# Optimization experiments

Measured on AMD Instinct MI355X. Metric: run time of the kernel, lower is better.

Reference implementation:

```python
import jax, jax.numpy as jnp
import numpy as np

B, TC, TP = 2, 1024, 512
NVC, NVP = 8, 4
D, K, H, DFF, L, HOR, NQ = 128, 3, 8, 512, 2, 96, 3
DK = D // H
MASK_VAL = -1e4  # finite stand-in for -inf; entmax15 support never reaches entries this far below the row max


def entmax15(z):
    # Exact 1.5-entmax over the last axis (Peters & Martins sort-based algorithm).
    z = z / 2.0
    z = z - jnp.max(z, axis=-1, keepdims=True)
    zs = jnp.flip(jnp.sort(z, axis=-1), axis=-1)  # descending
    kk = jnp.arange(1, z.shape[-1] + 1, dtype=z.dtype)
    mean = jnp.cumsum(zs, axis=-1) / kk
    meansq = jnp.cumsum(zs * zs, axis=-1) / kk
    ss = kk * (meansq - mean * mean)
    delta = (1.0 - ss) / kk
    pos = delta > 0
    sqrt_d = jnp.where(pos, jnp.sqrt(jnp.where(pos, delta, 1.0)), 0.0)  # grad-safe sqrt
    tau = mean - sqrt_d
    support = jnp.sum((tau <= zs).astype(jnp.int32), axis=-1, keepdims=True)
    tau_star = jnp.take_along_axis(tau, support - 1, axis=-1)
    return jnp.square(jnp.clip(z - tau_star, 0.0, None))


def layer_norm(x, g, b, eps=1e-5):
    m = jnp.mean(x, axis=-1, keepdims=True)
    v = jnp.mean(jnp.square(x - m), axis=-1, keepdims=True)
    return (x - m) * jax.lax.rsqrt(v + eps) * g + b


def selector(x, conv_w, conv_b, sel_w, sel_b, key):
    # x: [B, T, nv]; causal depthwise-grouped conv -> per-var local states [B, T, nv, D]
    Bs, T, nv = x.shape
    xc = jnp.transpose(x, (0, 2, 1))  # [B, nv, T]
    out = jax.lax.conv_general_dilated(
        xc, conv_w, window_strides=(1,), padding=[(K - 1, 0)],
        dimension_numbers=('NCH', 'OIH', 'NCH'), feature_group_count=nv)
    ls = out.reshape(Bs, nv, D, T) + conv_b[None, :, :, None]
    ls = jnp.transpose(ls, (0, 3, 1, 2))  # [B, T, nv, D]
    scores = ls @ sel_w + sel_b  # [B, T, nv]
    scores = jnp.clip(scores, -10.0, 10.0)
    scores = scores + 1e-4 * jax.random.normal(key, scores.shape, scores.dtype)
    w = entmax15(scores)  # [B, T, nv]
    weighted = jnp.sum(ls * w[..., None], axis=2)  # [B, T, D]
    return weighted, w


def attn_block(x, Wq, bq, Wk, bk, Wv, bv, Wo, bo):
    Bs, T, _ = x.shape
    q = (x @ Wq + bq).reshape(Bs, T, H, DK)
    k = (x @ Wk + bk).reshape(Bs, T, H, DK)
    v = (x @ Wv + bv).reshape(Bs, T, H, DK)
    scores = jnp.einsum('bthd,bshd->bhts', q, k) / jnp.sqrt(jnp.float32(DK))
    mask = jnp.triu(jnp.ones((T, T), bool), 1)
    scores = jnp.where(mask[None, None], MASK_VAL, scores)
    w = entmax15(scores)            # [B, H, T, T]
    w_avg = jnp.mean(w, axis=1)     # [B, T, T]
    v_comb = jnp.mean(v, axis=2)    # [B, T, DK]
    out = jnp.einsum('bts,bsd->btd', w_avg, v_comb)
    return out @ Wo + bo, w_avg


def forward(x_cond, x_pred, cw_c, cb_c, sw_c, sb_c, cw_p, cb_p, sw_p, sb_p,
            Wq, bq, Wk, bk, Wv, bv, Wo, bo, ln1_g, ln1_b,
            fw1, fb1, fw2, fb2, ln2_g, ln2_b, proj_w, proj_b):
    nk = jax.random.key(42)
    xc, v_cond = selector(x_cond, cw_c, cb_c, sw_c, sb_c, jax.random.fold_in(nk, 0))
    xp, v_pred = selector(x_pred, cw_p, cb_p, sw_p, sb_p, jax.random.fold_in(nk, 1))
    x = jnp.concatenate([xc, xp], axis=1)  # [B, TC+TP, D]
    logs = []
    for l in range(L):
        a, w = attn_block(x, Wq[l], bq[l], Wk[l], bk[l], Wv[l], bv[l], Wo[l], bo[l])
        x = layer_norm(x + a, ln1_g[l], ln1_b[l])
        h = jax.nn.relu(x @ fw1[l] + fb1[l])
        x = layer_norm(h @ fw2[l] + fb2[l] + x, ln2_g[l], ln2_b[l])
        logs.append(w)
    seq_last = x[:, -1, :]
    out = jnp.einsum('bd,qdh->bqh', seq_last, proj_w) + proj_b  # [B, NQ, HOR]
    return out, v_cond, v_pred, jnp.stack(logs)


def setup_inputs():
    key = jax.random.key(0)
    ks = jax.random.split(key, 16)
    def w(i, shp):
        return (0.02 * jax.random.normal(ks[i], shp)).astype(jnp.float32)
    z = lambda shp: jnp.zeros(shp, jnp.float32)
    o = lambda shp: jnp.ones(shp, jnp.float32)
    return {
        'x_cond': jax.random.normal(ks[0], (B, TC, NVC), jnp.float32),
        'x_pred': jax.random.normal(ks[1], (B, TP, NVP), jnp.float32),
        'cw_c': w(2, (NVC * D, 1, K)), 'cb_c': z((NVC, D)),
        'sw_c': w(3, (D,)), 'sb_c': z((1,)),
        'cw_p': w(4, (NVP * D, 1, K)), 'cb_p': z((NVP, D)),
        'sw_p': w(5, (D,)), 'sb_p': z((1,)),
        'Wq': w(6, (L, D, D)), 'bq': z((L, D)),
        'Wk': w(7, (L, D, D)), 'bk': z((L, D)),
        'Wv': w(8, (L, D, D)), 'bv': z((L, D)),
        'Wo': w(9, (L, DK, D)), 'bo': z((L, D)),
        'ln1_g': o((L, D)), 'ln1_b': z((L, D)),
        'fw1': w(10, (L, D, DFF)), 'fb1': z((L, DFF)),
        'fw2': w(11, (L, DFF, D)), 'fb2': z((L, D)),
        'ln2_g': o((L, D)), 'ln2_b': z((L, D)),
        'proj_w': w(12, (NQ, D, HOR)), 'proj_b': z((NQ, HOR)),
    }


def reference(x_cond, x_pred, cw_c, cb_c, sw_c, sb_c, cw_p, cb_p, sw_p, sb_p,
              Wq, bq, Wk, bk, Wv, bv, Wo, bo, ln1_g, ln1_b,
              fw1, fb1, fw2, fb2, ln2_g, ln2_b, proj_w, proj_b):
    return forward(x_cond, x_pred, cw_c, cb_c, sw_c, sb_c, cw_p, cb_p, sw_p, sb_p,
                   Wq, bq, Wk, bk, Wv, bv, Wo, bo, ln1_g, ln1_b,
                   fw1, fb1, fw2, fb2, ln2_g, ln2_b, proj_w, proj_b)
```

## Files before the change

kernel.cpp:

```cpp
#include <hip/hip_runtime.h>

namespace {

constexpr int NB_  = 2;
constexpr int TC_  = 1024;
constexpr int TP_  = 512;
constexpr int TT_  = 1536;
constexpr int D_   = 128;
constexpr int H_   = 8;
constexpr int DK_  = 16;
constexpr int DFF_ = 512;
constexpr int L_   = 2;
constexpr int HOR_ = 96;
constexpr int NQ_  = 3;

constexpr int SCP_ = TT_ + 8;

typedef _Float16 h2 __attribute__((ext_vector_type(2)));

constexpr int OFF_OUT  = 0;
constexpr int OFF_VC   = NB_ * NQ_ * HOR_;
constexpr int OFF_VP   = OFF_VC + NB_ * TC_ * 8;
constexpr int OFF_LOGS = OFF_VP + NB_ * TP_ * 4;

constexpr int WS_XA  = 0;
constexpr int WS_XB  = WS_XA  + NB_ * TT_ * D_;
constexpr int WS_Q16 = WS_XB  + NB_ * TT_ * D_;
constexpr int WS_K16 = WS_Q16 + NB_ * TT_ * D_ / 2;
constexpr int WS_VC  = WS_K16 + NB_ * TT_ * D_ / 2;
constexpr int WS_WVC = WS_VC  + NB_ * TT_ * DK_;
constexpr int WS_BVC = WS_WVC + L_ * D_ * DK_;

__device__ inline unsigned short f2bf(float x) {
    unsigned u = __float_as_uint(x);
    u = (u + 0x7fffu + ((u >> 16) & 1u)) >> 16;
    return (unsigned short)u;
}
__device__ inline float bf2f_lo(unsigned dw) { return __uint_as_float(dw << 16); }
__device__ inline float bf2f_hi(unsigned dw) { return __uint_as_float(dw & 0xffff0000u); }

__device__ inline float dot2f(h2 a, h2 b, float c) {
#if __has_builtin(__builtin_amdgcn_fdot2)
    return __builtin_amdgcn_fdot2(a, b, c, false);
#else
    return c + (float)a[0] * (float)b[0] + (float)a[1] * (float)b[1];
#endif
}

template <int NV>
__device__ inline void selector_body(
    const float* __restrict__ x, const float* __restrict__ cw,
    const float* __restrict__ cb, const float* __restrict__ sw,
    const float* __restrict__ sb, float* __restrict__ vout,
    float* __restrict__ xout, int Tsel, int row_off, int blk)
{
    const int b = blk / Tsel;
    const int t = blk - b * Tsel;
    const int d = threadIdx.x;
    const int lane = d & 63, wave = d >> 6;

    __shared__ float wsum[2][NV];
    __shared__ float wls[NV];

    float xw[3 * NV];
    #pragma unroll
    for (int kk = 0; kk < 3; ++kk) {
        const int ts = t + kk - 2;
        #pragma unroll
        for (int v = 0; v < NV; ++v)
            xw[kk * NV + v] = (ts >= 0) ? x[((long)b * Tsel + ts) * NV + v] : 0.0f;
    }

    float ls[NV];
    #pragma unroll
    for (int v = 0; v < NV; ++v) {
        const float* cwp = cw + ((long)(v * D_ + d)) * 3;
        float a = cb[v * D_ + d];
        a = fmaf(xw[0 * NV + v], cwp[0], a);
        a = fmaf(xw[1 * NV + v], cwp[1], a);
        a = fmaf(xw[2 * NV + v], cwp[2], a);
        ls[v] = a;
    }

    {
        const float swd = sw[d];
        float p[NV];
        #pragma unroll
        for (int v = 0; v < NV; ++v) p[v] = ls[v] * swd;
        #pragma unroll
        for (int off = 32; off; off >>= 1) {
            #pragma unroll
            for (int v = 0; v < NV; ++v) p[v] += __shfl_xor(p[v], off);
        }
        if (lane == 0) {
            #pragma unroll
            for (int v = 0; v < NV; ++v) wsum[wave][v] = p[v];
        }
    }
    __syncthreads();

    if (d == 0) {
        float u[NV];
        float m = -1e30f;
        #pragma unroll
        for (int v = 0; v < NV; ++v) {
            float s = wsum[0][v] + wsum[1][v] + sb[0];
            s = fminf(fmaxf(s, -10.0f), 10.0f);
            u[v] = 0.5f * s;
            m = fmaxf(m, u[v]);
        }
        float tau = m - 1.0f;
        for (int it = 0; it < 12; ++it) {
            float S1 = 0.f, S2 = 0.f;
            #pragma unroll
            for (int v = 0; v < NV; ++v) {
                float dd = fmaxf(u[v] - tau, 0.f);
                S1 += dd; S2 = fmaf(dd, dd, S2);
            }
            tau += (S2 - 1.0f) / (2.0f * S1);
        }
        {
            float S1 = 0.f, S2 = 0.f, K = 0.f;
            #pragma unroll
            for (int v = 0; v < NV; ++v) {
                if (u[v] > tau) { S1 += u[v]; S2 = fmaf(u[v], u[v], S2); K += 1.f; }
            }
            const float mean = S1 / K;
            const float arg  = fmaxf(fmaf(mean, mean, -(S2 - 1.0f) / K), 0.f);
            tau = mean - sqrtf(arg);
        }
        #pragma unroll
        for (int v = 0; v < NV; ++v) {
            float dd = fmaxf(u[v] - tau, 0.f);
            wls[v] = dd * dd;
        }
    }
    __syncthreads();

    float acc = 0.f;
    #pragma unroll
    for (int v = 0; v < NV; ++v) acc = fmaf(ls[v], wls[v], acc);
    xout[((long)b * TT_ + row_off + t) * D_ + d] = acc;
    if (d < NV) vout[((long)b * Tsel + t) * NV + d] = wls[d];
}

__device__ inline void prep_body(
    const float* __restrict__ Wv, const float* __restrict__ bv,
    float* __restrict__ wvc, float* __restrict__ bvc, int l)
{
    const float* W  = Wv + (long)l * D_ * D_;
    const float* bb = bv + l * D_;
    float* wv = wvc + l * D_ * DK_;
    float* bo = bvc + l * DK_;
    const int tid = threadIdx.x;
    for (int idx = tid; idx < D_ * DK_; idx += 128) {
        const int i = idx >> 4, dk = idx & 15;
        float s = 0.f;
        #pragma unroll
        for (int hh = 0; hh < H_; ++hh) s += W[i * D_ + hh * DK_ + dk];
        wv[idx] = s * 0.125f;
    }
    if (tid < DK_) {
        float s = 0.f;
        #pragma unroll
        for (int hh = 0; hh < H_; ++hh) s += bb[hh * DK_ + tid];
        bo[tid] = s * 0.125f;
    }
}

__global__ __launch_bounds__(128) void pre_kernel(
    const float* __restrict__ x_cond, const float* __restrict__ cw_c,
    const float* __restrict__ cb_c, const float* __restrict__ sw_c,
    const float* __restrict__ sb_c,
    const float* __restrict__ x_pred, const float* __restrict__ cw_p,
    const float* __restrict__ cb_p, const float* __restrict__ sw_p,
    const float* __restrict__ sb_p,
    const float* __restrict__ Wv, const float* __restrict__ bv,
    float* __restrict__ vc_out, float* __restrict__ vp_out,
    float* __restrict__ xout, float* __restrict__ wvc,
    float* __restrict__ bvc)
{
    const int blk = blockIdx.x;
    if (blk < NB_ * TC_) {
        selector_body<8>(x_cond, cw_c, cb_c, sw_c, sb_c, vc_out, xout,
                         TC_, 0, blk);
    } else if (blk < NB_ * TC_ + NB_ * TP_) {
        selector_body<4>(x_pred, cw_p, cb_p, sw_p, sb_p, vp_out, xout,
                         TP_, TC_, blk - NB_ * TC_);
    } else {
        prep_body(Wv, bv, wvc, bvc, blk - (NB_ * TC_ + NB_ * TP_));
    }
}

__global__ __launch_bounds__(256) void qkv_kernel(
    const float* __restrict__ x,
    const float* __restrict__ Wq, const float* __restrict__ bq,
    const float* __restrict__ Wk, const float* __restrict__ bk,
    const float* __restrict__ wvc, const float* __restrict__ bvc,
    _Float16* __restrict__ q16, _Float16* __restrict__ k16,
    float* __restrict__ vc)
{
    __shared__ float xrT[D_][4];
    const long row0 = (long)blockIdx.x * 4;
    const int tid = threadIdx.x;

    for (int idx = tid; idx < 4 * D_; idx += 256) {
        const int r = idx >> 7, i = idx & 127;
        xrT[i][r] = x[row0 * D_ + idx];
    }
    __syncthreads();

    const int c = tid & 127;
    const int which = tid >> 7;
    const float* __restrict__ W = which ? Wk : Wq;
    const float bb = which ? bk[c] : bq[c];
    float a0 = bb, a1 = bb, a2 = bb, a3 = bb;
    for (int i = 0; i < D_; ++i) {
        const float wv = W[i * D_ + c];
        const float4 xv = *(const float4*)&xrT[i][0];
        a0 = fmaf(xv.x, wv, a0);
        a1 = fmaf(xv.y, wv, a1);
        a2 = fmaf(xv.z, wv, a2);
        a3 = fmaf(xv.w, wv, a3);
    }
    _Float16* __restrict__ dst = which ? k16 : q16;
    dst[(row0 + 0) * D_ + c] = (_Float16)a0;
    dst[(row0 + 1) * D_ + c] = (_Float16)a1;
    dst[(row0 + 2) * D_ + c] = (_Float16)a2;
    dst[(row0 + 3) * D_ + c] = (_Float16)a3;

    if (tid < 64) {
        const int r = tid >> 4, c16 = tid & 15;
        float av = bvc[c16];
        for (int i = 0; i < D_; ++i)
            av = fmaf(xrT[i][r], wvc[i * DK_ + c16], av);
        vc[(row0 + r) * DK_ + c16] = av;
    }
}

template <int NJ>
__device__ inline void entmax_head(unsigned short* __restrict__ srow,
                                   int lane, int t)
{
    const unsigned* __restrict__ rp = (const unsigned*)srow;
    unsigned dw[NJ];
    #pragma unroll
    for (int j = 0; j < NJ; ++j) dw[j] = rp[64 * j + lane];
    float v[2 * NJ];
    #pragma unroll
    for (int j = 0; j < NJ; ++j) {
        const int s0 = 128 * j + 2 * lane;
        v[2*j]   = (s0     <= t) ? bf2f_lo(dw[j]) : -1e30f;
        v[2*j+1] = (s0 + 1 <= t) ? bf2f_hi(dw[j]) : -1e30f;
    }

    float m = -1e30f;
    #pragma unroll
    for (int j = 0; j < 2 * NJ; ++j) m = fmaxf(m, v[j]);
    #pragma unroll
    for (int off = 32; off; off >>= 1) m = fmaxf(m, __shfl_xor(m, off));

    float tau = m - 1.0f;
    #pragma unroll
    for (int it = 0; it < 7; ++it) {
        float S1 = 0.f, S2 = 0.f;
        #pragma unroll
        for (int j = 0; j < 2 * NJ; ++j) {
            const float d0 = fmaxf(v[j] - tau, 0.f);
            S1 += d0; S2 = fmaf(d0, d0, S2);
        }
        #pragma unroll
        for (int off = 32; off; off >>= 1) {
            S1 += __shfl_xor(S1, off);
            S2 += __shfl_xor(S2, off);
        }
        tau += (S2 - 1.0f) / (2.0f * S1);
    }
    {
        float S1 = 0.f, S2 = 0.f, K = 0.f;
        #pragma unroll
        for (int j = 0; j < 2 * NJ; ++j) {
            if (v[j] > tau) { S1 += v[j]; S2 = fmaf(v[j], v[j], S2); K += 1.f; }
        }
        #pragma unroll
        for (int off = 32; off; off >>= 1) {
            S1 += __shfl_xor(S1, off);
            S2 += __shfl_xor(S2, off);
            K  += __shfl_xor(K,  off);
        }
        const float mean = S1 / K;
        const float arg  = fmaxf(fmaf(mean, mean, -(S2 - 1.0f) / K), 0.f);
        tau = mean - sqrtf(arg);
    }
    unsigned* __restrict__ wp = (unsigned*)srow;
    #pragma unroll
    for (int j = 0; j < NJ; ++j) {
        const float d0 = fmaxf(v[2*j]   - tau, 0.f);
        const float d1 = fmaxf(v[2*j+1] - tau, 0.f);
        const unsigned lo = f2bf(d0 * d0);
        const unsigned hi = f2bf(d1 * d1);
        wp[64 * j + lane] = lo | (hi << 16);
    }
    #pragma unroll
    for (int j = NJ; j < 12; ++j) wp[64 * j + lane] = 0;
}

template <int NJ>
__device__ inline void entmax_pair(unsigned short* __restrict__ scb,
                                   int wave, int lane, int t)
{
    entmax_head<NJ>(scb + (wave * 2 + 0) * SCP_, lane, t);
    entmax_head<NJ>(scb + (wave * 2 + 1) * SCP_, lane, t);
}

__global__ __launch_bounds__(256) void attn_kernel(
    const _Float16* __restrict__ q16, const _Float16* __restrict__ k16,
    const float* __restrict__ vcomb, const float* __restrict__ xin,
    float* __restrict__ xout,
    const float* __restrict__ Wo, const float* __restrict__ bo,
    const float* __restrict__ lng, const float* __restrict__ lnb,
    float* __restrict__ logs)
{
    __shared__ unsigned short scb[H_ * SCP_];
    __shared__ _Float16 qrow16[D_];
    __shared__ float red[64];
    __shared__ float o16[DK_];
    __shared__ float yrow[D_];
    __shared__ float stat[2];

    const int blk = blockIdx.x;
    const int t = TT_ - 1 - (blk >> 1);
    const int b = blk & 1;
    const int tid = threadIdx.x;
    const int lane = tid & 63, wave = tid >> 6;
    const long rowq  = (long)b * TT_ + t;
    const long bbase = (long)b * TT_;

    if (tid < 64)
        ((unsigned*)qrow16)[tid] = ((const unsigned*)(q16 + rowq * D_))[tid];
    __syncthreads();

    {
        const int h  = tid & 7;
        const int sl = tid >> 3;
        unsigned short* __restrict__ srow = scb + h * SCP_;
        h2 qv[8];
        __builtin_memcpy(qv, (const _Float16*)qrow16 + h * DK_, 32);
        for (int s = sl; s <= t; s += 32) {
            float4 kk0, kk1;
            {
                const float4* kp4 = (const float4*)(k16 + (bbase + s) * D_ + h * DK_);
                kk0 = kp4[0]; kk1 = kp4[1];
            }
            h2 kh[8];
            __builtin_memcpy(kh,     &kk0, 16);
            __builtin_memcpy(kh + 4, &kk1, 16);
            float dot = 0.f;
            #pragma unroll
            for (int i2 = 0; i2 < 8; ++i2) dot = dot2f(qv[i2], kh[i2], dot);
            srow[s] = f2bf(dot * 0.125f);
        }
    }
    __syncthreads();

    {
        const int njn = (t >> 7) + 1;
        switch ((njn + 1) & ~1) {
        case 2:  entmax_pair<2 >(scb, wave, lane, t); break;
        case 4:  entmax_pair<4 >(scb, wave, lane, t); break;
        case 6:  entmax_pair<6 >(scb, wave, lane, t); break;
        case 8:  entmax_pair<8 >(scb, wave, lane, t); break;
        case 10: entmax_pair<10>(scb, wave, lane, t); break;
        default: entmax_pair<12>(scb, wave, lane, t); break;
        }
    }
    __syncthreads();

    float4 A0 = make_float4(0,0,0,0), A1 = A0, A2 = A0, A3 = A0;
    float* lrow = logs + rowq * TT_;
    const unsigned* __restrict__ rp0 = (const unsigned*)scb;
    #pragma unroll
    for (int it = 0; it < 3; ++it) {
        const int dwi = tid + 256 * it;
        const int s0 = 2 * dwi;
        if (s0 <= t) {
            float wa0 = 0.f, wa1 = 0.f;
            #pragma unroll
            for (int h = 0; h < H_; ++h) {
                const unsigned d = rp0[h * (SCP_ / 2) + dwi];
                wa0 += bf2f_lo(d);
                wa1 += bf2f_hi(d);
            }
            wa0 *= 0.125f; wa1 *= 0.125f;
            {
                const float4* vp = (const float4*)(vcomb + (bbase + s0) * DK_);
                const float4 v0 = vp[0], v1 = vp[1], v2 = vp[2], v3 = vp[3];
                A0.x = fmaf(wa0, v0.x, A0.x); A0.y = fmaf(wa0, v0.y, A0.y);
                A0.z = fmaf(wa0, v0.z, A0.z); A0.w = fmaf(wa0, v0.w, A0.w);
                A1.x = fmaf(wa0, v1.x, A1.x); A1.y = fmaf(wa0, v1.y, A1.y);
                A1.z = fmaf(wa0, v1.z, A1.z); A1.w = fmaf(wa0, v1.w, A1.w);
                A2.x = fmaf(wa0, v2.x, A2.x); A2.y = fmaf(wa0, v2.y, A2.y);
                A2.z = fmaf(wa0, v2.z, A2.z); A2.w = fmaf(wa0, v2.w, A2.w);
                A3.x = fmaf(wa0, v3.x, A3.x); A3.y = fmaf(wa0, v3.y, A3.y);
                A3.z = fmaf(wa0, v3.z, A3.z); A3.w = fmaf(wa0, v3.w, A3.w);
            }
            if (s0 + 1 <= t) {
                const float4* vp = (const float4*)(vcomb + (bbase + s0 + 1) * DK_);
                const float4 v0 = vp[0], v1 = vp[1], v2 = vp[2], v3 = vp[3];
                A0.x = fmaf(wa1, v0.x, A0.x); A0.y = fmaf(wa1, v0.y, A0.y);
                A0.z = fmaf(wa1, v0.z, A0.z); A0.w = fmaf(wa1, v0.w, A0.w);
                A1.x = fmaf(wa1, v1.x, A1.x); A1.y = fmaf(wa1, v1.y, A1.y);
                A1.z = fmaf(wa1, v1.z, A1.z); A1.w = fmaf(wa1, v1.w, A1.w);
                A2.x = fmaf(wa1, v2.x, A2.x); A2.y = fmaf(wa1, v2.y, A2.y);
                A2.z = fmaf(wa1, v2.z, A2.z); A2.w = fmaf(wa1, v2.w, A2.w);
                A3.x = fmaf(wa1, v3.x, A3.x); A3.y = fmaf(wa1, v3.y, A3.y);
                A3.z = fmaf(wa1, v3.z, A3.z); A3.w = fmaf(wa1, v3.w, A3.w);
            }
            *(float2*)(lrow + s0) = make_float2(wa0, wa1);
        } else {
            *(float2*)(lrow + s0) = make_float2(0.f, 0.f);
        }
    }
    #pragma unroll
    for (int off = 32; off; off >>= 1) {
        A0.x += __shfl_xor(A0.x, off); A0.y += __shfl_xor(A0.y, off);
        A0.z += __shfl_xor(A0.z, off); A0.w += __shfl_xor(A0.w, off);
        A1.x += __shfl_xor(A1.x, off); A1.y += __shfl_xor(A1.y, off);
        A1.z += __shfl_xor(A1.z, off); A1.w += __shfl_xor(A1.w, off);
        A2.x += __shfl_xor(A2.x, off); A2.y += __shfl_xor(A2.y, off);
        A2.z += __shfl_xor(A2.z, off); A2.w += __shfl_xor(A2.w, off);
        A3.x += __shfl_xor(A3.x, off); A3.y += __shfl_xor(A3.y, off);
        A3.z += __shfl_xor(A3.z, off); A3.w += __shfl_xor(A3.w, off);
    }
    if (lane == 0) {
        float* r = red + wave * 16;
        r[0]=A0.x; r[1]=A0.y; r[2]=A0.z; r[3]=A0.w;
        r[4]=A1.x; r[5]=A1.y; r[6]=A1.z; r[7]=A1.w;
        r[8]=A2.x; r[9]=A2.y; r[10]=A2.z; r[11]=A2.w;
        r[12]=A3.x; r[13]=A3.y; r[14]=A3.z; r[15]=A3.w;
    }
    __syncthreads();
    if (tid < DK_) o16[tid] = red[tid] + red[16 + tid] + red[32 + tid] + red[48 + tid];
    __syncthreads();

    float y = 0.f;
    if (tid < D_) {
        float a = bo[tid];
        #pragma unroll
        for (int j = 0; j < DK_; ++j) a = fmaf(o16[j], Wo[j * D_ + tid], a);
        y = xin[rowq * D_ + tid] + a;
        yrow[tid] = y;
    }
    __syncthreads();
    if (tid < 64) {
        float sm = yrow[tid] + yrow[tid + 64];
        #pragma unroll
        for (int off = 32; off; off >>= 1) sm += __shfl_xor(sm, off);
        if (tid == 0) stat[0] = sm * (1.0f / D_);
    }
    __syncthreads();
    if (tid < 64) {
        const float mean = stat[0];
        const float d0 = yrow[tid] - mean, d1 = yrow[tid + 64] - mean;
        float sv = fmaf(d0, d0, d1 * d1);
        #pragma unroll
        for (int off = 32; off; off >>= 1) sv += __shfl_xor(sv, off);
        if (tid == 0) stat[1] = sv * (1.0f / D_);
    }
    __syncthreads();
    if (tid < D_) {
        const float r = rsqrtf(stat[1] + 1e-5f);
        xout[rowq * D_ + tid] = (y - stat[0]) * r * lng[tid] + lnb[tid];
    }
}

__global__ __launch_bounds__(256) void ffn_kernel(
    const float* __restrict__ xin, float* __restrict__ xout,
    const float* __restrict__ fw1, const float* __restrict__ fb1,
    const float* __restrict__ fw2, const float* __restrict__ fb2,
    const float* __restrict__ g, const float* __restrict__ bta,
    int do_proj, const float* __restrict__ pw,
    const float* __restrict__ pb, float* __restrict__ outp)
{
    __shared__ float xrT[D_][4];
    __shared__ float hbT[DFF_][4];
    __shared__ float yb[4][D_];
    __shared__ float xn[D_];

    const long row0 = (long)blockIdx.x * 4;
    const int tid = threadIdx.x;

    for (int idx = tid; idx < 4 * D_; idx += 256) {
        const int r = idx >> 7, i = idx & 127;
        xrT[i][r] = xin[row0 * D_ + idx];
    }
    __syncthreads();

    {
        const int c = tid;
        float4 a0 = make_float4(0,0,0,0), a1 = a0;
        for (int i = 0; i < D_; ++i) {
            const float w0 = fw1[i * DFF_ + c];
            const float w1 = fw1[i * DFF_ + c + 256];
            const float4 xv = *(const float4*)&xrT[i][0];
            a0.x = fmaf(xv.x, w0, a0.x); a0.y = fmaf(xv.y, w0, a0.y);
            a0.z = fmaf(xv.z, w0, a0.z); a0.w = fmaf(xv.w, w0, a0.w);
            a1.x = fmaf(xv.x, w1, a1.x); a1.y = fmaf(xv.y, w1, a1.y);
            a1.z = fmaf(xv.z, w1, a1.z); a1.w = fmaf(xv.w, w1, a1.w);
        }
        const float b0 = fb1[c], b1 = fb1[c + 256];
        float4 h0, h1;
        h0.x = fmaxf(a0.x + b0, 0.f); h0.y = fmaxf(a0.y + b0, 0.f);
        h0.z = fmaxf(a0.z + b0, 0.f); h0.w = fmaxf(a0.w + b0, 0.f);
        h1.x = fmaxf(a1.x + b1, 0.f); h1.y = fmaxf(a1.y + b1, 0.f);
        h1.z = fmaxf(a1.z + b1, 0.f); h1.w = fmaxf(a1.w + b1, 0.f);
        *(float4*)&hbT[c][0]       = h0;
        *(float4*)&hbT[c + 256][0] = h1;
    }
    __syncthreads();

    {
        const int d = tid & 127;
        const int r0 = (tid >> 7) * 2;
        float a0 = 0.f, a1 = 0.f;
        for (int j = 0; j < DFF_; ++j) {
            const float wv = fw2[j * D_ + d];
            const float2 hv = *(const float2*)&hbT[j][r0];
            a0 = fmaf(hv.x, wv, a0);
            a1 = fmaf(hv.y, wv, a1);
        }
        const float bb = fb2[d];
        yb[r0 + 0][d] = a0 + bb + xrT[d][r0 + 0];
        yb[r0 + 1][d] = a1 + bb + xrT[d][r0 + 1];
    }
    __syncthreads();

    const int w = tid >> 6, lane = tid & 63;
    const bool pblk = do_proj && (((row0 + 4) % TT_) == 0);
    {
        const float y0 = yb[w][lane], y1 = yb[w][lane + 64];
        float sm = y0 + y1;
        #pragma unroll
        for (int off = 32; off; off >>= 1) sm += __shfl_xor(sm, off);
        const float mean = sm * (1.0f / D_);
        const float d0 = y0 - mean, d1 = y1 - mean;
        float sv = fmaf(d0, d0, d1 * d1);
        #pragma unroll
        for (int off = 32; off; off >>= 1) sv += __shfl_xor(sv, off);
        const float rcp = rsqrtf(sv * (1.0f / D_) + 1e-5f);
        const float o0 = d0 * rcp * g[lane]      + bta[lane];
        const float o1 = d1 * rcp * g[lane + 64] + bta[lane + 64];
        xout[(row0 + w) * D_ + lane]      = o0;
        xout[(row0 + w) * D_ + lane + 64] = o1;
        if (pblk && w == 3) { xn[lane] = o0; xn[lane + 64] = o1; }
    }
    if (pblk) {
        __syncthreads();
        const int b = (int)((row0 + 3) / TT_);
        for (int idx = tid; idx < NQ_ * HOR_; idx += 256) {
            const int qq = idx / HOR_, hh = idx - qq * HOR_;
            float s = pb[idx];
            for (int d = 0; d < D_; ++d)
                s = fmaf(xn[d], pw[((long)qq * D_ + d) * HOR_ + hh], s);
            outp[b * NQ_ * HOR_ + idx] = s;
        }
    }
}

}

extern "C" void kernel_launch(void* const* d_in, const int* in_sizes, int n_in,
                              void* d_out, int out_size, void* d_ws, size_t ws_size,
                              hipStream_t stream) {
    (void)in_sizes; (void)n_in; (void)out_size; (void)ws_size;

    const float* x_cond = (const float*)d_in[0];
    const float* x_pred = (const float*)d_in[1];
    const float* cw_c   = (const float*)d_in[2];
    const float* cb_c   = (const float*)d_in[3];
    const float* sw_c   = (const float*)d_in[4];
    const float* sb_c   = (const float*)d_in[5];
    const float* cw_p   = (const float*)d_in[6];
    const float* cb_p   = (const float*)d_in[7];
    const float* sw_p   = (const float*)d_in[8];
    const float* sb_p   = (const float*)d_in[9];
    const float* Wq     = (const float*)d_in[10];
    const float* bq     = (const float*)d_in[11];
    const float* Wk     = (const float*)d_in[12];
    const float* bk     = (const float*)d_in[13];
    const float* Wv     = (const float*)d_in[14];
    const float* bv     = (const float*)d_in[15];
    const float* Wo     = (const float*)d_in[16];
    const float* bo     = (const float*)d_in[17];
    const float* ln1g   = (const float*)d_in[18];
    const float* ln1b   = (const float*)d_in[19];
    const float* fw1    = (const float*)d_in[20];
    const float* fb1    = (const float*)d_in[21];
    const float* fw2    = (const float*)d_in[22];
    const float* fb2    = (const float*)d_in[23];
    const float* ln2g   = (const float*)d_in[24];
    const float* ln2b   = (const float*)d_in[25];
    const float* pw     = (const float*)d_in[26];
    const float* pb     = (const float*)d_in[27];

    float* outp = (float*)d_out;
    float* ws   = (float*)d_ws;
    float*     xA   = ws + WS_XA;
    float*     xB   = ws + WS_XB;
    _Float16*  q16  = (_Float16*)(ws + WS_Q16);
    _Float16*  k16  = (_Float16*)(ws + WS_K16);
    float*     vcb  = ws + WS_VC;
    float*     wvc  = ws + WS_WVC;
    float*     bvc  = ws + WS_BVC;

    pre_kernel<<<NB_ * TC_ + NB_ * TP_ + L_, 128, 0, stream>>>(
        x_cond, cw_c, cb_c, sw_c, sb_c,
        x_pred, cw_p, cb_p, sw_p, sb_p,
        Wv, bv, outp + OFF_VC, outp + OFF_VP, xA, wvc, bvc);

    for (int l = 0; l < L_; ++l) {
        qkv_kernel<<<NB_ * TT_ / 4, 256, 0, stream>>>(
            xA, Wq + (long)l * D_ * D_, bq + l * D_,
            Wk + (long)l * D_ * D_, bk + l * D_,
            wvc + l * D_ * DK_, bvc + l * DK_, q16, k16, vcb);
        attn_kernel<<<NB_ * TT_, 256, 0, stream>>>(
            q16, k16, vcb, xA, xB,
            Wo + (long)l * DK_ * D_, bo + l * D_,
            ln1g + l * D_, ln1b + l * D_,
            outp + OFF_LOGS + (long)l * NB_ * TT_ * TT_);
        ffn_kernel<<<NB_ * TT_ / 4, 256, 0, stream>>>(
            xB, xA, fw1 + (long)l * D_ * DFF_, fb1 + l * DFF_,
            fw2 + (long)l * DFF_ * D_, fb2 + l * D_,
            ln2g + l * D_, ln2b + l * D_,
            (l == L_ - 1) ? 1 : 0, pw, pb, outp);
    }
}
```

Measured before the change: 342.1 us.

## Fuse QKV projection into selector and FFN kernels, dropping qkv_kernel launches

Removes the standalone qkv_kernel. The layer-0 Q/K/V projection now runs at the tail of the selector kernel, one row per block. The next layer's projection now runs at the tail of the FFN kernel, reusing the LayerNorm output already staged in shared memory. The Wv head-averaging prep moves into its own tiny kernel so the selector can depend on it. This saves launches and a re-read of the activations, but the selector path now reads the full Wq/Wk once per row instead of once per four rows, which lowers weight reuse.

```diff
diff --git a/kernel.cpp b/kernel.cpp
--- a/kernel.cpp
+++ b/kernel.cpp
@@ -47,12 +47,42 @@
 #endif
 }
 
+__global__ __launch_bounds__(128) void prep_wvc_kernel(
+    const float* __restrict__ Wv, const float* __restrict__ bv,
+    float* __restrict__ wvc, float* __restrict__ bvc)
+{
+    const int l = blockIdx.x;
+    const float* W  = Wv + (long)l * D_ * D_;
+    const float* bb = bv + l * D_;
+    float* wv = wvc + l * D_ * DK_;
+    float* bo = bvc + l * DK_;
+    const int tid = threadIdx.x;
+    for (int idx = tid; idx < D_ * DK_; idx += 128) {
+        const int i = idx >> 4, dk = idx & 15;
+        float s = 0.f;
+        #pragma unroll
+        for (int hh = 0; hh < H_; ++hh) s += W[i * D_ + hh * DK_ + dk];
+        wv[idx] = s * 0.125f;
+    }
+    if (tid < DK_) {
+        float s = 0.f;
+        #pragma unroll
+        for (int hh = 0; hh < H_; ++hh) s += bb[hh * DK_ + tid];
+        bo[tid] = s * 0.125f;
+    }
+}
+
 template <int NV>
 __device__ inline void selector_body(
     const float* __restrict__ x, const float* __restrict__ cw,
     const float* __restrict__ cb, const float* __restrict__ sw,
     const float* __restrict__ sb, float* __restrict__ vout,
-    float* __restrict__ xout, int Tsel, int row_off, int blk)
+    float* __restrict__ xout, int Tsel, int row_off, int blk,
+    const float* __restrict__ Wq, const float* __restrict__ bq,
+    const float* __restrict__ Wk, const float* __restrict__ bk,
+    const float* __restrict__ wvc, const float* __restrict__ bvc,
+    _Float16* __restrict__ q16, _Float16* __restrict__ k16,
+    float* __restrict__ vc)
 {
     const int b = blk / Tsel;
     const int t = blk - b * Tsel;
@@ -61,6 +91,8 @@
 
     __shared__ float wsum[2][NV];
     __shared__ float wls[NV];
+    __shared__ float xr[D_];
+    __shared__ float vred[DK_][8];
 
     float xw[3 * NV];
     #pragma unroll
@@ -140,31 +172,36 @@
     float acc = 0.f;
     #pragma unroll
     for (int v = 0; v < NV; ++v) acc = fmaf(ls[v], wls[v], acc);
-    xout[((long)b * TT_ + row_off + t) * D_ + d] = acc;
+    const long row = (long)b * TT_ + row_off + t;
+    xout[row * D_ + d] = acc;
     if (d < NV) vout[((long)b * Tsel + t) * NV + d] = wls[d];
-}
-
-__device__ inline void prep_body(
-    const float* __restrict__ Wv, const float* __restrict__ bv,
-    float* __restrict__ wvc, float* __restrict__ bvc, int l)
-{
-    const float* W  = Wv + (long)l * D_ * D_;
-    const float* bb = bv + l * D_;
-    float* wv = wvc + l * D_ * DK_;
-    float* bo = bvc + l * DK_;
-    const int tid = threadIdx.x;
-    for (int idx = tid; idx < D_ * DK_; idx += 128) {
-        const int i = idx >> 4, dk = idx & 15;
-        float s = 0.f;
-        #pragma unroll
-        for (int hh = 0; hh < H_; ++hh) s += W[i * D_ + hh * DK_ + dk];
-        wv[idx] = s * 0.125f;
-    }
-    if (tid < DK_) {
-        float s = 0.f;
-        #pragma unroll
-        for (int hh = 0; hh < H_; ++hh) s += bb[hh * DK_ + tid];
-        bo[tid] = s * 0.125f;
+
+    xr[d] = acc;
+    __syncthreads();
+
+    float aq = bq[d], ak = bk[d];
+    for (int i = 0; i < D_; ++i) {
+        const float xv = xr[i];
+        aq = fmaf(xv, Wq[i * D_ + d], aq);
+        ak = fmaf(xv, Wk[i * D_ + d], ak);
+    }
+    q16[row * D_ + d] = (_Float16)aq;
+    k16[row * D_ + d] = (_Float16)ak;
+
+    {
+        const int dk = d & 15, ch = d >> 4;
+        float p = 0.f;
+        #pragma unroll
+        for (int i = 0; i < 16; ++i)
+            p = fmaf(xr[ch * 16 + i], wvc[(ch * 16 + i) * DK_ + dk], p);
+        vred[dk][ch] = p;
+    }
+    __syncthreads();
+    if (d < DK_) {
+        float s = bvc[d];
+        #pragma unroll
+        for (int ch = 0; ch < 8; ++ch) s += vred[d][ch];
+        vc[row * DK_ + d] = s;
     }
 }
 
@@ -175,66 +212,22 @@
     const float* __restrict__ x_pred, const float* __restrict__ cw_p,
     const float* __restrict__ cb_p, const float* __restrict__ sw_p,
     const float* __restrict__ sb_p,
-    const float* __restrict__ Wv, const float* __restrict__ bv,
     float* __restrict__ vc_out, float* __restrict__ vp_out,
-    float* __restrict__ xout, float* __restrict__ wvc,
-    float* __restrict__ bvc)
-{
-    const int blk = blockIdx.x;
-    if (blk < NB_ * TC_) {
-        selector_body<8>(x_cond, cw_c, cb_c, sw_c, sb_c, vc_out, xout,
-                         TC_, 0, blk);
-    } else if (blk < NB_ * TC_ + NB_ * TP_) {
-        selector_body<4>(x_pred, cw_p, cb_p, sw_p, sb_p, vp_out, xout,
-                         TP_, TC_, blk - NB_ * TC_);
-    } else {
-        prep_body(Wv, bv, wvc, bvc, blk - (NB_ * TC_ + NB_ * TP_));
-    }
-}
-
-__global__ __launch_bounds__(256) void qkv_kernel(
-    const float* __restrict__ x,
+    float* __restrict__ xout,
     const float* __restrict__ Wq, const float* __restrict__ bq,
     const float* __restrict__ Wk, const float* __restrict__ bk,
     const float* __restrict__ wvc, const float* __restrict__ bvc,
     _Float16* __restrict__ q16, _Float16* __restrict__ k16,
     float* __restrict__ vc)
 {
-    __shared__ float xrT[D_][4];
-    const long row0 = (long)blockIdx.x * 4;
-    const int tid = threadIdx.x;
-
-    for (int idx = tid; idx < 4 * D_; idx += 256) {
-        const int r = idx >> 7, i = idx & 127;
-        xrT[i][r] = x[row0 * D_ + idx];
-    }
-    __syncthreads();
-
-    const int c = tid & 127;
-    const int which = tid >> 7;
-    const float* __restrict__ W = which ? Wk : Wq;
-    const float bb = which ? bk[c] : bq[c];
-    float a0 = bb, a1 = bb, a2 = bb, a3 = bb;
-    for (int i = 0; i < D_; ++i) {
-        const float wv = W[i * D_ + c];
-        const float4 xv = *(const float4*)&xrT[i][0];
-        a0 = fmaf(xv.x, wv, a0);
-        a1 = fmaf(xv.y, wv, a1);
-        a2 = fmaf(xv.z, wv, a2);
-        a3 = fmaf(xv.w, wv, a3);
-    }
-    _Float16* __restrict__ dst = which ? k16 : q16;
-    dst[(row0 + 0) * D_ + c] = (_Float16)a0;
-    dst[(row0 + 1) * D_ + c] = (_Float16)a1;
-    dst[(row0 + 2) * D_ + c] = (_Float16)a2;
-    dst[(row0 + 3) * D_ + c] = (_Float16)a3;
-
-    if (tid < 64) {
-        const int r = tid >> 4, c16 = tid & 15;
-        float av = bvc[c16];
-        for (int i = 0; i < D_; ++i)
-            av = fmaf(xrT[i][r], wvc[i * DK_ + c16], av);
-        vc[(row0 + r) * DK_ + c16] = av;
+    const int blk = blockIdx.x;
+    if (blk < NB_ * TC_) {
+        selector_body<8>(x_cond, cw_c, cb_c, sw_c, sb_c, vc_out, xout,
+                         TC_, 0, blk, Wq, bq, Wk, bk, wvc, bvc, q16, k16, vc);
+    } else {
+        selector_body<4>(x_pred, cw_p, cb_p, sw_p, sb_p, vp_out, xout,
+                         TP_, TC_, blk - NB_ * TC_,
+                         Wq, bq, Wk, bk, wvc, bvc, q16, k16, vc);
     }
 }
 
@@ -479,6 +472,12 @@
     const float* __restrict__ fw1, const float* __restrict__ fb1,
     const float* __restrict__ fw2, const float* __restrict__ fb2,
     const float* __restrict__ g, const float* __restrict__ bta,
+    int do_qkv,
+    const float* __restrict__ Wq, const float* __restrict__ bq,
+    const float* __restrict__ Wk, const float* __restrict__ bk,
+    const float* __restrict__ wvc, const float* __restrict__ bvc,
+    _Float16* __restrict__ q16, _Float16* __restrict__ k16,
+    float* __restrict__ vc,
     int do_proj, const float* __restrict__ pw,
     const float* __restrict__ pb, float* __restrict__ outp)
 {
@@ -552,8 +551,41 @@
         const float o1 = d1 * rcp * g[lane + 64] + bta[lane + 64];
         xout[(row0 + w) * D_ + lane]      = o0;
         xout[(row0 + w) * D_ + lane + 64] = o1;
+        xrT[lane][w]      = o0;
+        xrT[lane + 64][w] = o1;
         if (pblk && w == 3) { xn[lane] = o0; xn[lane + 64] = o1; }
     }
+
+    if (do_qkv) {
+        __syncthreads();
+        const int c = tid & 127;
+        const int which = tid >> 7;
+        const float* __restrict__ W = which ? Wk : Wq;
+        const float bb = which ? bk[c] : bq[c];
+        float a0 = bb, a1 = bb, a2 = bb, a3 = bb;
+        for (int i = 0; i < D_; ++i) {
+            const float wv = W[i * D_ + c];
+            const float4 xv = *(const float4*)&xrT[i][0];
+            a0 = fmaf(xv.x, wv, a0);
+            a1 = fmaf(xv.y, wv, a1);
+            a2 = fmaf(xv.z, wv, a2);
+            a3 = fmaf(xv.w, wv, a3);
+        }
+        _Float16* __restrict__ dst = which ? k16 : q16;
+        dst[(row0 + 0) * D_ + c] = (_Float16)a0;
+        dst[(row0 + 1) * D_ + c] = (_Float16)a1;
+        dst[(row0 + 2) * D_ + c] = (_Float16)a2;
+        dst[(row0 + 3) * D_ + c] = (_Float16)a3;
+
+        if (tid < 64) {
+            const int r = tid >> 4, c16 = tid & 15;
+            float av = bvc[c16];
+            for (int i = 0; i < D_; ++i)
+                av = fmaf(xrT[i][r], wvc[i * DK_ + c16], av);
+            vc[(row0 + r) * DK_ + c16] = av;
+        }
+    }
+
     if (pblk) {
         __syncthreads();
         const int b = (int)((row0 + 3) / TT_);
@@ -613,25 +645,33 @@
     float*     wvc  = ws + WS_WVC;
     float*     bvc  = ws + WS_BVC;
 
-    pre_kernel<<<NB_ * TC_ + NB_ * TP_ + L_, 128, 0, stream>>>(
+    prep_wvc_kernel<<<L_, 128, 0, stream>>>(Wv, bv, wvc, bvc);
+
+    pre_kernel<<<NB_ * TC_ + NB_ * TP_, 128, 0, stream>>>(
         x_cond, cw_c, cb_c, sw_c, sb_c,
         x_pred, cw_p, cb_p, sw_p, sb_p,
-        Wv, bv, outp + OFF_VC, outp + OFF_VP, xA, wvc, bvc);
+        outp + OFF_VC, outp + OFF_VP, xA,
+        Wq, bq, Wk, bk, wvc, bvc, q16, k16, vcb);
 
     for (int l = 0; l < L_; ++l) {
-        qkv_kernel<<<NB_ * TT_ / 4, 256, 0, stream>>>(
-            xA, Wq + (long)l * D_ * D_, bq + l * D_,
-            Wk + (long)l * D_ * D_, bk + l * D_,
-            wvc + l * D_ * DK_, bvc + l * DK_, q16, k16, vcb);
         attn_kernel<<<NB_ * TT_, 256, 0, stream>>>(
             q16, k16, vcb, xA, xB,
             Wo + (long)l * DK_ * D_, bo + l * D_,
             ln1g + l * D_, ln1b + l * D_,
             outp + OFF_LOGS + (long)l * NB_ * TT_ * TT_);
+        const int nl = l + 1;
         ffn_kernel<<<NB_ * TT_ / 4, 256, 0, stream>>>(
             xB, xA, fw1 + (long)l * D_ * DFF_, fb1 + l * DFF_,
             fw2 + (long)l * DFF_ * D_, fb2 + l * D_,
             ln2g + l * D_, ln2b + l * D_,
+            (l < L_ - 1) ? 1 : 0,
+            Wq + (long)nl * D_ * D_ * (l < L_ - 1),
+            bq + nl * D_ * (l < L_ - 1),
+            Wk + (long)nl * D_ * D_ * (l < L_ - 1),
+            bk + nl * D_ * (l < L_ - 1),
+            wvc + nl * D_ * DK_ * (l < L_ - 1),
+            bvc + nl * DK_ * (l < L_ - 1),
+            q16, k16, vcb,
             (l == L_ - 1) ? 1 : 0, pw, pb, outp);
     }
 }
```

New measurement: 341.6 us. No clear change (-0.2%).
